# Kernel tuning notes

Measured on AMD Instinct MI355X. Metric: run time of the kernel, lower is better.

The kernel has to match this reference:

```python
import jax, jax.numpy as jnp
import numpy as np

BASE_CHUNK = 64
MAX_SEQ_LEN = 256
HIDDEN = 128
DIST_CORE = 6.0
DIST_SHELL = 10.0


def _linear_params(key, fan_in, fan_out):
    lim = 1.0 / np.sqrt(fan_in)
    kw, kb = jax.random.split(key)
    W = jax.random.uniform(kw, (fan_in, fan_out), jnp.float32, -lim, lim)
    b = jax.random.uniform(kb, (fan_out,), jnp.float32, -lim, lim)
    return W, b


def setup_inputs() -> dict:
    key = jax.random.key(0)
    ks = jax.random.split(key, 8)
    B, S, De = 16, 768, 16
    node_features = jax.random.normal(ks[0], (B, S, HIDDEN), jnp.float32)
    # channel 0 acts as a pairwise distance; uniform in [0, 20) spans core/shell thresholds
    edge_features = jax.random.uniform(ks[1], (B, S, S, De), jnp.float32) * 20.0
    sequence_mask = jnp.ones((B, S), jnp.float32)
    pocket_mask = jax.random.bernoulli(ks[2], 0.02, (B, S))
    W_node, b_node = _linear_params(ks[3], HIDDEN, 32)
    W_e1, b_e1 = _linear_params(ks[4], 1, 64)
    W_e2, b_e2 = _linear_params(ks[5], 64, 32)
    W_imp, b_imp = _linear_params(ks[6], 64, 1)
    return dict(node_features=node_features, edge_features=edge_features,
                sequence_mask=sequence_mask, pocket_mask=pocket_mask,
                W_node=W_node, b_node=b_node, W_e1=W_e1, b_e1=b_e1,
                W_e2=W_e2, b_e2=b_e2, W_imp=W_imp, b_imp=b_imp)


def reference(node_features, edge_features, sequence_mask, pocket_mask,
              W_node, b_node, W_e1, b_e1, W_e2, b_e2, W_imp, b_imp):
    B, S, _ = node_features.shape
    adj = min(BASE_CHUNK, MAX_SEQ_LEN // 4) if S > MAX_SEQ_LEN else BASE_CHUNK  # static

    node_enc = node_features @ W_node + b_node                      # [B,S,32]
    edge_summary = edge_features.mean(axis=-1).mean(axis=-1)[..., None]  # [B,S,1]
    h = jax.nn.relu(edge_summary @ W_e1 + b_e1)                     # [B,S,64]
    edge_enc = h @ W_e2 + b_e2                                      # [B,S,32]
    combined = jnp.concatenate([node_enc, edge_enc], axis=-1)       # [B,S,64]
    importance = jax.nn.sigmoid(combined @ W_imp + b_imp) * sequence_mask[..., None]  # [B,S,1]
    imp = importance[..., 0]                                        # [B,S]

    # ---- pocket branch (vectorized over batch) ----
    # min distance from each node to any pocket node (inf where no pocket)
    dist = jnp.where(pocket_mask[:, None, :], edge_features[..., 0], jnp.inf).min(axis=2)  # [B,S]
    core = dist < DIST_CORE
    imp_mean = imp.mean(axis=1, keepdims=True)
    shell = (dist >= DIST_CORE) & (dist < DIST_SHELL) & (imp > imp_mean)
    merged = pocket_mask | core | shell
    merged_len = jnp.minimum(merged.sum(axis=1), MAX_SEQ_LEN)       # clamp (argsort path keeps max_seq_len)
    chunk_pocket = jnp.minimum(jnp.maximum(merged_len, adj), MAX_SEQ_LEN).astype(jnp.float32)

    # ---- no-pocket branch ----
    imp_full = importance.mean(axis=(1, 2))                          # [B]
    chunk_np = jnp.clip(BASE_CHUNK * imp_full,
                        float(adj // 2), float(min(adj * 2, MAX_SEQ_LEN)))

    has_pocket = pocket_mask.any(axis=1)
    chunk_sizes = jnp.where(has_pocket, chunk_pocket, chunk_np)      # [B]
    return chunk_sizes, MAX_SEQ_LEN
```

## Files before the change

kernel.cpp:

```cpp
#include <hip/hip_runtime.h>
#include <hip/hip_bf16.h>
#include <math.h>

#define BB 16
#define SS 768
#define DE 16
#define HID 128


__global__ __launch_bounds__(256) void sniff_kernel(const unsigned int* __restrict__ pm,
                                                    int* __restrict__ flag) {
    __shared__ int bad;
    int tid = threadIdx.x;
    if (tid == 0) bad = 0;
    __syncthreads();
    for (int t = tid; t < (BB * SS) / 4; t += 256) {
        unsigned int w = pm[t];
        if (w > 1u && w != 0x3F800000u) bad = 1;
    }
    __syncthreads();
    if (tid == 0) *flag = bad;
}

__global__ __launch_bounds__(128) void precompute_kernel(
    const float* __restrict__ Wn, const float* __restrict__ bn,
    const float* __restrict__ We2, const float* __restrict__ be2,
    const float* __restrict__ Wimp, const float* __restrict__ bimp,
    float* __restrict__ ws) {
    int tid = threadIdx.x;
    if (tid < 128) {
        float s = 0.f;
        for (int c = 0; c < 32; ++c) s += Wn[tid * 32 + c] * Wimp[c];
        ws[16 + tid] = s;
    }
    if (tid < 64) {
        float s = 0.f;
        for (int c = 0; c < 32; ++c) s += We2[tid * 32 + c] * Wimp[32 + c];
        ws[144 + tid] = s;
    }
    if (tid == 0) {
        float s = bimp[0];
        for (int c = 0; c < 32; ++c) s += bn[c] * Wimp[c];
        for (int c = 0; c < 32; ++c) s += be2[c] * Wimp[32 + c];
        ws[208] = s;
    }
}

__global__ __launch_bounds__(256) void edge_kernel(
    const float4* __restrict__ edge, const float* __restrict__ nf,
    const void* __restrict__ pmask, const float* __restrict__ seqmask,
    const float* __restrict__ We1, const float* __restrict__ be1,
    float* __restrict__ ws) {
    const int tid = threadIdx.x;
    const int bi = blockIdx.x;
    const int b = bi / SS;

    __shared__ float s_a[256];
    __shared__ float s_b[256];
    __shared__ unsigned char s_m[SS];

    const int flag = ((const int*)ws)[0];
    if (flag) {
        const unsigned char* pm = (const unsigned char*)pmask + (size_t)b * SS;
        for (int j = tid; j < SS; j += 256) s_m[j] = pm[j] ? 1 : 0;
    } else {
        const unsigned int* pm = (const unsigned int*)pmask + (size_t)b * SS;
        for (int j = tid; j < SS; j += 256) s_m[j] = pm[j] ? 1 : 0;
    }
    __syncthreads();

    const float4* row = edge + (size_t)bi * (SS * DE / 4);
    float sum = 0.f;
    float dmin = INFINITY;
#pragma unroll
    for (int it = 0; it < 12; ++it) {
        int t = tid + it * 256;
        float4 v = row[t];
        sum += (v.x + v.y) + (v.z + v.w);
        if ((t & 3) == 0) {
            if (s_m[t >> 2]) dmin = fminf(dmin, v.x);
        }
    }
    s_a[tid] = sum;
    s_b[tid] = dmin;
    __syncthreads();
    for (int off = 128; off > 0; off >>= 1) {
        if (tid < off) {
            s_a[tid] += s_a[tid + off];
            s_b[tid] = fminf(s_b[tid], s_b[tid + off]);
        }
        __syncthreads();
    }
    const float total = s_a[0];
    const float dall = s_b[0];
    __syncthreads();

    const float es = total * (1.0f / (float)(SS * DE));
    float p = 0.f;
    if (tid < 128) p += nf[(size_t)bi * HID + tid] * ws[16 + tid];
    if (tid < 64) {
        float h = es * We1[tid] + be1[tid];
        h = fmaxf(h, 0.f);
        p += h * ws[144 + tid];
    }
    s_a[tid] = p;
    __syncthreads();
    for (int off = 128; off > 0; off >>= 1) {
        if (tid < off) s_a[tid] += s_a[tid + off];
        __syncthreads();
    }
    if (tid == 0) {
        float logit = s_a[0] + ws[208];
        float impv = seqmask[bi] / (1.f + expf(-logit));
        ws[256 + bi] = impv;
        ws[256 + BB * SS + bi] = dall;
    }
}

__global__ __launch_bounds__(256) void final_kernel(
    const void* __restrict__ pmask, const float* __restrict__ ws,
    float* __restrict__ out) {
    const int tid = threadIdx.x;
    const int b = blockIdx.x;
    __shared__ float s_f[256];
    __shared__ int s_i[256];

    const float* imp = ws + 256;
    const float* dist = ws + 256 + BB * SS;
    const int flag = ((const int*)ws)[0];

    float psum = 0.f;
    int por = 0;
    for (int i = tid; i < SS; i += 256) {
        psum += imp[b * SS + i];
        int m = flag ? (((const unsigned char*)pmask)[b * SS + i] != 0)
                     : (((const unsigned int*)pmask)[b * SS + i] != 0u);
        por |= m;
    }
    s_f[tid] = psum;
    s_i[tid] = por;
    __syncthreads();
    for (int off = 128; off > 0; off >>= 1) {
        if (tid < off) {
            s_f[tid] += s_f[tid + off];
            s_i[tid] |= s_i[tid + off];
        }
        __syncthreads();
    }
    const float imp_mean = s_f[0] / (float)SS;
    const int haspocket = s_i[0];
    __syncthreads();

    int cnt = 0;
    for (int i = tid; i < SS; i += 256) {
        int m = flag ? (((const unsigned char*)pmask)[b * SS + i] != 0)
                     : (((const unsigned int*)pmask)[b * SS + i] != 0u);
        float d = dist[b * SS + i];
        bool core = d < 6.0f;
        bool shell = (d >= 6.0f) && (d < 10.0f) && (imp[b * SS + i] > imp_mean);
        cnt += (m || core || shell) ? 1 : 0;
    }
    s_i[tid] = cnt;
    __syncthreads();
    for (int off = 128; off > 0; off >>= 1) {
        if (tid < off) s_i[tid] += s_i[tid + off];
        __syncthreads();
    }
    if (tid == 0) {
        float chunk;
        if (haspocket) {
            float ml = fminf((float)s_i[0], 256.f);
            chunk = fminf(fmaxf(ml, 64.f), 256.f);
        } else {
            chunk = fminf(fmaxf(64.f * imp_mean, 32.f), 128.f);
        }
        out[b] = chunk;
        if (b == 0) out[BB] = 256.f;
    }
}

extern "C" void kernel_launch(void* const* d_in, const int* in_sizes, int n_in,
                              void* d_out, int out_size, void* d_ws, size_t ws_size,
                              hipStream_t stream) {
    const float* nf = (const float*)d_in[0];
    const float4* edge = (const float4*)d_in[1];
    const float* seqmask = (const float*)d_in[2];
    const void* pmask = d_in[3];
    const float* Wn = (const float*)d_in[4];
    const float* bn = (const float*)d_in[5];
    const float* We1 = (const float*)d_in[6];
    const float* be1 = (const float*)d_in[7];
    const float* We2 = (const float*)d_in[8];
    const float* be2 = (const float*)d_in[9];
    const float* Wimp = (const float*)d_in[10];
    const float* bimp = (const float*)d_in[11];
    float* ws = (float*)d_ws;
    float* out = (float*)d_out;

    sniff_kernel<<<1, 256, 0, stream>>>((const unsigned int*)pmask, (int*)ws);
    precompute_kernel<<<1, 128, 0, stream>>>(Wn, bn, We2, be2, Wimp, bimp, ws);
    edge_kernel<<<BB * SS, 256, 0, stream>>>(edge, nf, pmask, seqmask, We1, be1, ws);
    final_kernel<<<BB, 256, 0, stream>>>(pmask, ws, out);
}
```

Measured before the change: 786.0 us.

## Map one wavefront per edge row with shuffle reductions; merge setup kernels

The edge kernel now assigns one 64-lane wavefront to each (batch, node) row, four rows per block. Shared-memory tree reductions with many __syncthreads are replaced by wavefront shuffle reductions. The pocket-mask sniff and weight precompute kernels are merged into one two-block launch to save a launch. The change removes block-level sync overhead in a memory-bound streaming kernel, but each lane now issues more loads in sequence.

New measurement: 798.3 us. About the same (+1.6%).

```diff
diff --git a/kernel.cpp b/kernel.cpp
--- a/kernel.cpp
+++ b/kernel.cpp
@@ -8,41 +8,40 @@
 #define HID 128
 
 
-__global__ __launch_bounds__(256) void sniff_kernel(const unsigned int* __restrict__ pm,
-                                                    int* __restrict__ flag) {
-    __shared__ int bad;
-    int tid = threadIdx.x;
-    if (tid == 0) bad = 0;
-    __syncthreads();
-    for (int t = tid; t < (BB * SS) / 4; t += 256) {
-        unsigned int w = pm[t];
-        if (w > 1u && w != 0x3F800000u) bad = 1;
-    }
-    __syncthreads();
-    if (tid == 0) *flag = bad;
-}
-
-__global__ __launch_bounds__(128) void precompute_kernel(
+__global__ __launch_bounds__(256) void setup_kernel(
+    const unsigned int* __restrict__ pm,
     const float* __restrict__ Wn, const float* __restrict__ bn,
     const float* __restrict__ We2, const float* __restrict__ be2,
     const float* __restrict__ Wimp, const float* __restrict__ bimp,
     float* __restrict__ ws) {
-    int tid = threadIdx.x;
-    if (tid < 128) {
-        float s = 0.f;
-        for (int c = 0; c < 32; ++c) s += Wn[tid * 32 + c] * Wimp[c];
-        ws[16 + tid] = s;
-    }
-    if (tid < 64) {
-        float s = 0.f;
-        for (int c = 0; c < 32; ++c) s += We2[tid * 32 + c] * Wimp[32 + c];
-        ws[144 + tid] = s;
-    }
-    if (tid == 0) {
-        float s = bimp[0];
-        for (int c = 0; c < 32; ++c) s += bn[c] * Wimp[c];
-        for (int c = 0; c < 32; ++c) s += be2[c] * Wimp[32 + c];
-        ws[208] = s;
+    const int tid = threadIdx.x;
+    if (blockIdx.x == 0) {
+        __shared__ int bad;
+        if (tid == 0) bad = 0;
+        __syncthreads();
+        for (int t = tid; t < (BB * SS) / 4; t += 256) {
+            unsigned int w = pm[t];
+            if (w > 1u && w != 0x3F800000u) bad = 1;
+        }
+        __syncthreads();
+        if (tid == 0) ((int*)ws)[0] = bad;
+    } else {
+        if (tid < 128) {
+            float s = 0.f;
+            for (int c = 0; c < 32; ++c) s += Wn[tid * 32 + c] * Wimp[c];
+            ws[16 + tid] = s;
+        }
+        if (tid < 64) {
+            float s = 0.f;
+            for (int c = 0; c < 32; ++c) s += We2[tid * 32 + c] * Wimp[32 + c];
+            ws[144 + tid] = s;
+        }
+        if (tid == 0) {
+            float s = bimp[0];
+            for (int c = 0; c < 32; ++c) s += bn[c] * Wimp[c];
+            for (int c = 0; c < 32; ++c) s += be2[c] * Wimp[32 + c];
+            ws[208] = s;
+        }
     }
 }
 
@@ -52,13 +51,12 @@
     const float* __restrict__ We1, const float* __restrict__ be1,
     float* __restrict__ ws) {
     const int tid = threadIdx.x;
-    const int bi = blockIdx.x;
-    const int b = bi / SS;
+    const int lane = tid & 63;
+    const int wid = tid >> 6;
+    const int bi = blockIdx.x * 4 + wid;
+    const int b = blockIdx.x / (SS / 4);
 
-    __shared__ float s_a[256];
-    __shared__ float s_b[256];
     __shared__ unsigned char s_m[SS];
-
     const int flag = ((const int*)ws)[0];
     if (flag) {
         const unsigned char* pm = (const unsigned char*)pmask + (size_t)b * SS;
@@ -69,51 +67,41 @@
     }
     __syncthreads();
 
+    const float nf0 = nf[(size_t)bi * HID + lane];
+    const float nf1 = nf[(size_t)bi * HID + 64 + lane];
+
     const float4* row = edge + (size_t)bi * (SS * DE / 4);
     float sum = 0.f;
     float dmin = INFINITY;
-#pragma unroll
-    for (int it = 0; it < 12; ++it) {
-        int t = tid + it * 256;
-        float4 v = row[t];
+    const bool ch0 = (lane & 3) == 0;
+    const int j0 = lane >> 2;
+#pragma unroll 8
+    for (int k = 0; k < 48; ++k) {
+        float4 v = row[lane + (k << 6)];
         sum += (v.x + v.y) + (v.z + v.w);
-        if ((t & 3) == 0) {
-            if (s_m[t >> 2]) dmin = fminf(dmin, v.x);
+        if (ch0) {
+            if (s_m[j0 + (k << 4)]) dmin = fminf(dmin, v.x);
         }
     }
-    s_a[tid] = sum;
-    s_b[tid] = dmin;
-    __syncthreads();
-    for (int off = 128; off > 0; off >>= 1) {
-        if (tid < off) {
-            s_a[tid] += s_a[tid + off];
-            s_b[tid] = fminf(s_b[tid], s_b[tid + off]);
-        }
-        __syncthreads();
+
+#pragma unroll
+    for (int m = 32; m > 0; m >>= 1) {
+        sum += __shfl_xor(sum, m, 64);
+        dmin = fminf(dmin, __shfl_xor(dmin, m, 64));
     }
-    const float total = s_a[0];
-    const float dall = s_b[0];
-    __syncthreads();
 
-    const float es = total * (1.0f / (float)(SS * DE));
-    float p = 0.f;
-    if (tid < 128) p += nf[(size_t)bi * HID + tid] * ws[16 + tid];
-    if (tid < 64) {
-        float h = es * We1[tid] + be1[tid];
-        h = fmaxf(h, 0.f);
-        p += h * ws[144 + tid];
-    }
-    s_a[tid] = p;
-    __syncthreads();
-    for (int off = 128; off > 0; off >>= 1) {
-        if (tid < off) s_a[tid] += s_a[tid + off];
-        __syncthreads();
-    }
-    if (tid == 0) {
-        float logit = s_a[0] + ws[208];
+    const float es = sum * (1.0f / (float)(SS * DE));
+    float p = nf0 * ws[16 + lane] + nf1 * ws[16 + 64 + lane];
+    float h = fmaxf(es * We1[lane] + be1[lane], 0.f);
+    p += h * ws[144 + lane];
+#pragma unroll
+    for (int m = 32; m > 0; m >>= 1) p += __shfl_xor(p, m, 64);
+
+    if (lane == 0) {
+        float logit = p + ws[208];
         float impv = seqmask[bi] / (1.f + expf(-logit));
         ws[256 + bi] = impv;
-        ws[256 + BB * SS + bi] = dall;
+        ws[256 + BB * SS + bi] = dmin;
     }
 }
 
@@ -197,8 +185,8 @@
     float* ws = (float*)d_ws;
     float* out = (float*)d_out;
 
-    sniff_kernel<<<1, 256, 0, stream>>>((const unsigned int*)pmask, (int*)ws);
-    precompute_kernel<<<1, 128, 0, stream>>>(Wn, bn, We2, be2, Wimp, bimp, ws);
-    edge_kernel<<<BB * SS, 256, 0, stream>>>(edge, nf, pmask, seqmask, We1, be1, ws);
+    setup_kernel<<<2, 256, 0, stream>>>((const unsigned int*)pmask,
+                                        Wn, bn, We2, be2, Wimp, bimp, ws);
+    edge_kernel<<<(BB * SS) / 4, 256, 0, stream>>>(edge, nf, pmask, seqmask, We1, be1, ws);
     final_kernel<<<BB, 256, 0, stream>>>(pmask, ws, out);
 }
```
